# Optimization experiments

Measured on AMD Instinct MI355X. Metric: run time of the kernel, lower is better.

Reference implementation:

```python
import jax, jax.numpy as jnp
import numpy as np

STRIDE = 1
PADDING = 1  # zeros padding mode

def setup_inputs() -> dict:
    key = jax.random.key(0)
    k1, k2, k3 = jax.random.split(key, 3)
    N, C_in, H, W = 32, 128, 56, 56
    C_out, kH, kW = 256, 3, 3
    x = jax.random.normal(k1, (N, C_in, H, W), dtype=jnp.float32)
    fan_in = C_in * kH * kW
    weight = jax.random.normal(k2, (C_out, C_in, kH, kW), dtype=jnp.float32) / np.sqrt(fan_in)
    bias = jax.random.normal(k3, (C_out,), dtype=jnp.float32) * 0.01
    return {"x": x, "weight": weight, "bias": bias}

def reference(x, weight, bias):
    # Same math as the im2col unfold + GEMM: a standard 2D cross-correlation
    # with zero padding. Expressed as the fused implicit-GEMM conv primitive.
    out = jax.lax.conv_general_dilated(
        x, weight,
        window_strides=(STRIDE, STRIDE),
        padding=[(PADDING, PADDING), (PADDING, PADDING)],
        dimension_numbers=("NCHW", "OIHW", "NCHW"),
    )
    # bias broadcast over (N, C_out, H_out, W_out)
    return out + bias[None, :, None, None]
```

## Files before the change

### kernel.cpp

```cpp
#include <hip/hip_runtime.h>


typedef __attribute__((ext_vector_type(8))) short short8;
typedef __attribute__((ext_vector_type(4))) float float4v;

constexpr int NB = 32, CI = 128, HH = 56, WW = 56, CO = 256;
constexpr int HWP = HH * WW;
constexpr int M_TOTAL = NB * HWP;
constexpr size_t XT_BYTES = (size_t)NB * HWP * CI * 2;
constexpr size_t WT_BYTES = (size_t)9 * CO * CI * 2;
constexpr size_t ZP_OFF   = XT_BYTES + WT_BYTES;
constexpr size_t WS_NEED  = ZP_OFF + 128;

__device__ inline ushort f2bf(float v) {
    union { float f; uint u; } c; c.f = v;
    uint u = c.u;
    return (ushort)((u + 0x7fffu + ((u >> 16) & 1u)) >> 16);
}

__global__ __launch_bounds__(256) void xform_x(const float* __restrict__ x,
                                               ushort* __restrict__ xT) {
    int b = blockIdx.x;
    int cit = b & 3;
    int hwt = (b >> 2) % 49;
    int n   = b / (4 * 49);
    int ci0 = cit * 32, hw0 = hwt * 64;
    __shared__ float t[32][65];
    int tx = threadIdx.x;
    int col = tx & 63, r4 = tx >> 6;
#pragma unroll
    for (int rr = 0; rr < 8; ++rr) {
        int row = rr * 4 + r4;
        t[row][col] = x[((size_t)n * CI + ci0 + row) * HWP + hw0 + col];
    }
    __syncthreads();
    int i = tx & 31, j0 = tx >> 5;
#pragma unroll
    for (int jj = 0; jj < 8; ++jj) {
        int j = jj * 8 + j0;
        xT[((size_t)n * HWP + hw0 + j) * CI + ci0 + i] = f2bf(t[i][j]);
    }
}

__global__ __launch_bounds__(256) void xform_w(const float* __restrict__ w,
                                               ushort* __restrict__ wT) {
    int o = blockIdx.x * 256 + threadIdx.x;
    int ci = o & 127;
    int co = (o >> 7) & 255;
    int tap = o >> 15;
    wT[o] = f2bf(w[((size_t)co * CI + ci) * 9 + tap]);
}

__global__ __launch_bounds__(256) void gemm_conv(
    const ushort* __restrict__ xT, const ushort* __restrict__ wT,
    const ushort* __restrict__ zp, const float* __restrict__ bias,
    float* __restrict__ out)
{
    __shared__ ushort As[128 * 64];
    __shared__ ushort Bs[128 * 64];

    const int mblk = blockIdx.x >> 1;
    const int cblk = blockIdx.x & 1;
    const int tid = threadIdx.x, lane = tid & 63, wv = tid >> 6;
    const int wco = wv >> 1, wm = wv & 1;
    const int s = (lane & 7) ^ ((lane >> 3) & 7);

    int ho_[4], wo_[4], mpix[4], rowW[4];
#pragma unroll
    for (int q = 0; q < 4; ++q) {
        int r = wv * 32 + q * 8 + (lane >> 3);
        rowW[q] = r;
        int m = mblk * 128 + r;
        mpix[q] = m;
        int hw = m % HWP;
        ho_[q] = hw / WW;
        wo_[q] = hw % WW;
    }

    float4v acc[4][4];
#pragma unroll
    for (int i = 0; i < 4; ++i)
#pragma unroll
        for (int j = 0; j < 4; ++j) acc[i][j] = (float4v)(0.0f);

    for (int tap = 0; tap < 9; ++tap) {
        const int dh = tap / 3 - 1, dw = tap % 3 - 1;
        for (int cb = 0; cb < 2; ++cb) {
#pragma unroll
            for (int q = 0; q < 4; ++q) {
                const ushort* g = wT + ((size_t)tap * CO + cblk * 128 + rowW[q]) * CI
                                     + cb * 64 + s * 8;
                __builtin_amdgcn_global_load_lds(
                    (const __attribute__((address_space(1))) uint*)g,
                    (__attribute__((address_space(3))) uint*)(As + (wv * 32 + q * 8) * 64),
                    16, 0, 0);
            }
#pragma unroll
            for (int q = 0; q < 4; ++q) {
                int hi = ho_[q] + dh, wi = wo_[q] + dw;
                bool ok = (hi >= 0) & (hi < HH) & (wi >= 0) & (wi < WW);
                const ushort* g = ok
                    ? (xT + ((size_t)(mpix[q] + dh * WW + dw)) * CI + cb * 64 + s * 8)
                    : (zp + (lane & 7) * 8);
                __builtin_amdgcn_global_load_lds(
                    (const __attribute__((address_space(1))) uint*)g,
                    (__attribute__((address_space(3))) uint*)(Bs + (wv * 32 + q * 8) * 64),
                    16, 0, 0);
            }
            __syncthreads();
#pragma unroll
            for (int kk = 0; kk < 2; ++kk) {
                short8 a[4], b[4];
#pragma unroll
                for (int f = 0; f < 4; ++f) {
                    int row = wco * 64 + f * 16 + (lane & 15);
                    int ch = (kk * 4 + (lane >> 4)) ^ (row & 7);
                    a[f] = *(const short8*)(As + row * 64 + ch * 8);
                }
#pragma unroll
                for (int f = 0; f < 4; ++f) {
                    int row = wm * 64 + f * 16 + (lane & 15);
                    int ch = (kk * 4 + (lane >> 4)) ^ (row & 7);
                    b[f] = *(const short8*)(Bs + row * 64 + ch * 8);
                }
#pragma unroll
                for (int i = 0; i < 4; ++i)
#pragma unroll
                    for (int j = 0; j < 4; ++j)
                        acc[i][j] = __builtin_amdgcn_mfma_f32_16x16x32_bf16(
                            a[i], b[j], acc[i][j], 0, 0, 0);
            }
            __syncthreads();
        }
    }

    const int co0 = cblk * 128 + wco * 64;
    const int m0  = mblk * 128 + wm * 64;
    float bv[4][4];
#pragma unroll
    for (int i = 0; i < 4; ++i)
#pragma unroll
        for (int r = 0; r < 4; ++r)
            bv[i][r] = bias[co0 + i * 16 + (lane >> 4) * 4 + r];
#pragma unroll
    for (int j = 0; j < 4; ++j) {
        int m = m0 + j * 16 + (lane & 15);
        int n = m / HWP, hw = m % HWP;
        float* obase = out + (size_t)n * CO * HWP + hw;
#pragma unroll
        for (int i = 0; i < 4; ++i) {
            int co = co0 + i * 16 + (lane >> 4) * 4;
#pragma unroll
            for (int r = 0; r < 4; ++r)
                obase[(size_t)(co + r) * HWP] = acc[i][j][r] + bv[i][r];
        }
    }
}

__global__ __launch_bounds__(256) void conv_k(
    const float* __restrict__ x, const float* __restrict__ wgt,
    const float* __restrict__ bias, float* __restrict__ out)
{
    int idx = blockIdx.x * 256 + threadIdx.x;
    int wg = idx % 14; int t = idx / 14;
    int ho = t % 56; t /= 56;
    int cog = t % 64; int n = t / 64;
    int w0 = wg * 4, co0 = cog * 4;
    float acc[4][4];
#pragma unroll
    for (int j = 0; j < 4; ++j) {
        float bj = bias[co0 + j];
#pragma unroll
        for (int p = 0; p < 4; ++p) acc[j][p] = bj;
    }
    const float* xn = x + (size_t)n * CI * HWP;
    for (int ci = 0; ci < CI; ++ci) {
        float xr[3][6];
#pragma unroll
        for (int kh = 0; kh < 3; ++kh) {
            int hi = ho + kh - 1;
            if (hi >= 0 && hi < HH) {
                const float* row = xn + ((size_t)ci * HH + hi) * WW;
                float4 c = *reinterpret_cast<const float4*>(row + w0);
                xr[kh][1] = c.x; xr[kh][2] = c.y; xr[kh][3] = c.z; xr[kh][4] = c.w;
                xr[kh][0] = (w0 > 0) ? row[w0 - 1] : 0.0f;
                xr[kh][5] = (w0 + 4 < WW) ? row[w0 + 4] : 0.0f;
            } else {
#pragma unroll
                for (int q = 0; q < 6; ++q) xr[kh][q] = 0.0f;
            }
        }
#pragma unroll
        for (int j = 0; j < 4; ++j) {
            const float* wp = wgt + ((size_t)(co0 + j) * CI + ci) * 9;
            float wvv[9];
#pragma unroll
            for (int q = 0; q < 9; ++q) wvv[q] = wp[q];
#pragma unroll
            for (int kh = 0; kh < 3; ++kh)
#pragma unroll
                for (int kw = 0; kw < 3; ++kw)
#pragma unroll
                    for (int p = 0; p < 4; ++p)
                        acc[j][p] = fmaf(xr[kh][p + kw], wvv[kh * 3 + kw], acc[j][p]);
        }
    }
#pragma unroll
    for (int j = 0; j < 4; ++j) {
        float4 v = make_float4(acc[j][0], acc[j][1], acc[j][2], acc[j][3]);
        *reinterpret_cast<float4*>(out + (((size_t)n * CO + co0 + j) * HH + ho) * WW + w0) = v;
    }
}

extern "C" void kernel_launch(void* const* d_in, const int* in_sizes, int n_in,
                              void* d_out, int out_size, void* d_ws, size_t ws_size,
                              hipStream_t stream) {
    const float* x = (const float*)d_in[0];
    const float* w = (const float*)d_in[1];
    const float* b = (const float*)d_in[2];
    float* out = (float*)d_out;

    if (ws_size < WS_NEED) {
        hipLaunchKernelGGL(conv_k, dim3(6272), dim3(256), 0, stream, x, w, b, out);
        return;
    }

    ushort* xT = (ushort*)d_ws;
    ushort* wT = (ushort*)((char*)d_ws + XT_BYTES);
    ushort* zp = (ushort*)((char*)d_ws + ZP_OFF);

    hipMemsetAsync(zp, 0, 128, stream);
    hipLaunchKernelGGL(xform_x, dim3(32 * 49 * 4), dim3(256), 0, stream, x, xT);
    hipLaunchKernelGGL(xform_w, dim3(9 * CO * CI / 256), dim3(256), 0, stream, w, wT);
    hipLaunchKernelGGL(gemm_conv, dim3(784 * 2), dim3(256), 0, stream,
                       xT, wT, zp, b, out);
}
```

Before: 104.6 us.

## Pre-pad input in NHWC bf16 layout and remap block order for cache locality

The transposed bf16 input is now written into a zero-bordered 58x58 buffer, and a new kernel zeroes that border. The GEMM loop can then drop its per-tap bounds checks and zero-page fallback, using precomputed offsets instead. The block index is also remapped so each group of 8 consecutive blocks is strided across the grid, and the loops are reordered to iterate taps inside channel halves. These changes cost one extra small launch and a slightly larger workspace, and the remap may affect L2 reuse of neighbouring pixel rows.

```diff
diff --git a/kernel.cpp b/kernel.cpp
--- a/kernel.cpp
+++ b/kernel.cpp
@@ -6,11 +6,11 @@
 
 constexpr int NB = 32, CI = 128, HH = 56, WW = 56, CO = 256;
 constexpr int HWP = HH * WW;
-constexpr int M_TOTAL = NB * HWP;
-constexpr size_t XT_BYTES = (size_t)NB * HWP * CI * 2;
-constexpr size_t WT_BYTES = (size_t)9 * CO * CI * 2;
-constexpr size_t ZP_OFF   = XT_BYTES + WT_BYTES;
-constexpr size_t WS_NEED  = ZP_OFF + 128;
+constexpr int HP = 58, WP = 58;
+constexpr size_t XTP_BYTES = (size_t)NB * HP * WP * CI * 2;
+constexpr size_t WT_OFF    = XTP_BYTES;
+constexpr size_t WT_BYTES  = (size_t)9 * CO * CI * 2;
+constexpr size_t WS_NEED   = WT_OFF + WT_BYTES;
 
 __device__ inline ushort f2bf(float v) {
     union { float f; uint u; } c; c.f = v;
@@ -19,7 +19,7 @@
 }
 
 __global__ __launch_bounds__(256) void xform_x(const float* __restrict__ x,
-                                               ushort* __restrict__ xT) {
+                                               ushort* __restrict__ xTp) {
     int b = blockIdx.x;
     int cit = b & 3;
     int hwt = (b >> 2) % 49;
@@ -38,8 +38,23 @@
 #pragma unroll
     for (int jj = 0; jj < 8; ++jj) {
         int j = jj * 8 + j0;
-        xT[((size_t)n * HWP + hw0 + j) * CI + ci0 + i] = f2bf(t[i][j]);
-    }
+        int hw = hw0 + j;
+        int h = hw / WW, w = hw % WW;
+        xTp[(((size_t)n * HP + h + 1) * WP + (w + 1)) * CI + ci0 + i] = f2bf(t[i][j]);
+    }
+}
+
+__global__ __launch_bounds__(256) void xform_border(ushort* __restrict__ xTp) {
+    int u = blockIdx.x * 256 + threadIdx.x;
+    int ci8 = u & 15;
+    int r = u >> 4;
+    int n = r / 228, bb = r % 228;
+    int hp, wp;
+    if (bb < 58)       { hp = 0;  wp = bb; }
+    else if (bb < 116) { hp = 57; wp = bb - 58; }
+    else { int c = bb - 116; hp = 1 + (c >> 1); wp = (c & 1) * 57; }
+    short8 z = (short8)0;
+    *reinterpret_cast<short8*>(xTp + (((size_t)n * HP + hp) * WP + wp) * CI + ci8 * 8) = z;
 }
 
 __global__ __launch_bounds__(256) void xform_w(const float* __restrict__ w,
@@ -52,29 +67,29 @@
 }
 
 __global__ __launch_bounds__(256) void gemm_conv(
-    const ushort* __restrict__ xT, const ushort* __restrict__ wT,
-    const ushort* __restrict__ zp, const float* __restrict__ bias,
-    float* __restrict__ out)
+    const ushort* __restrict__ xTp, const ushort* __restrict__ wT,
+    const float* __restrict__ bias, float* __restrict__ out)
 {
     __shared__ ushort As[128 * 64];
     __shared__ ushort Bs[128 * 64];
 
-    const int mblk = blockIdx.x >> 1;
-    const int cblk = blockIdx.x & 1;
+    int b = blockIdx.x;
+    int logical = (b & 7) * 196 + (b >> 3);
+    const int mblk = logical >> 1;
+    const int cblk = logical & 1;
+
     const int tid = threadIdx.x, lane = tid & 63, wv = tid >> 6;
     const int wco = wv >> 1, wm = wv & 1;
     const int s = (lane & 7) ^ ((lane >> 3) & 7);
 
-    int ho_[4], wo_[4], mpix[4], rowW[4];
+    int aOff[4], bOff[4];
 #pragma unroll
     for (int q = 0; q < 4; ++q) {
         int r = wv * 32 + q * 8 + (lane >> 3);
-        rowW[q] = r;
+        aOff[q] = (cblk * 128 + r) * CI + s * 8;
         int m = mblk * 128 + r;
-        mpix[q] = m;
-        int hw = m % HWP;
-        ho_[q] = hw / WW;
-        wo_[q] = hw % WW;
+        int n = m / HWP, hw = m % HWP, h = hw / WW, w = hw % WW;
+        bOff[q] = ((n * HP + h + 1) * WP + (w + 1)) * CI + s * 8;
     }
 
     float4v acc[4][4];
@@ -83,34 +98,30 @@
 #pragma unroll
         for (int j = 0; j < 4; ++j) acc[i][j] = (float4v)(0.0f);
 
-    for (int tap = 0; tap < 9; ++tap) {
-        const int dh = tap / 3 - 1, dw = tap % 3 - 1;
-        for (int cb = 0; cb < 2; ++cb) {
+    for (int cb = 0; cb < 2; ++cb) {
+#pragma unroll 1
+        for (int tap = 0; tap < 9; ++tap) {
+            const int dh = tap / 3 - 1, dw = tap % 3 - 1;
+            const int toff = (dh * WP + dw) * CI + cb * 64;
+            const int atap = tap * CO * CI + cb * 64;
 #pragma unroll
             for (int q = 0; q < 4; ++q) {
-                const ushort* g = wT + ((size_t)tap * CO + cblk * 128 + rowW[q]) * CI
-                                     + cb * 64 + s * 8;
                 __builtin_amdgcn_global_load_lds(
-                    (const __attribute__((address_space(1))) uint*)g,
+                    (const __attribute__((address_space(1))) uint*)(wT + aOff[q] + atap),
                     (__attribute__((address_space(3))) uint*)(As + (wv * 32 + q * 8) * 64),
                     16, 0, 0);
             }
 #pragma unroll
             for (int q = 0; q < 4; ++q) {
-                int hi = ho_[q] + dh, wi = wo_[q] + dw;
-                bool ok = (hi >= 0) & (hi < HH) & (wi >= 0) & (wi < WW);
-                const ushort* g = ok
-                    ? (xT + ((size_t)(mpix[q] + dh * WW + dw)) * CI + cb * 64 + s * 8)
-                    : (zp + (lane & 7) * 8);
                 __builtin_amdgcn_global_load_lds(
-                    (const __attribute__((address_space(1))) uint*)g,
+                    (const __attribute__((address_space(1))) uint*)(xTp + bOff[q] + toff),
                     (__attribute__((address_space(3))) uint*)(Bs + (wv * 32 + q * 8) * 64),
                     16, 0, 0);
             }
             __syncthreads();
 #pragma unroll
             for (int kk = 0; kk < 2; ++kk) {
-                short8 a[4], b[4];
+                short8 a[4], bfr[4];
 #pragma unroll
                 for (int f = 0; f < 4; ++f) {
                     int row = wco * 64 + f * 16 + (lane & 15);
@@ -121,14 +132,14 @@
                 for (int f = 0; f < 4; ++f) {
                     int row = wm * 64 + f * 16 + (lane & 15);
                     int ch = (kk * 4 + (lane >> 4)) ^ (row & 7);
-                    b[f] = *(const short8*)(Bs + row * 64 + ch * 8);
+                    bfr[f] = *(const short8*)(Bs + row * 64 + ch * 8);
                 }
 #pragma unroll
                 for (int i = 0; i < 4; ++i)
 #pragma unroll
                     for (int j = 0; j < 4; ++j)
                         acc[i][j] = __builtin_amdgcn_mfma_f32_16x16x32_bf16(
-                            a[i], b[j], acc[i][j], 0, 0, 0);
+                            a[i], bfr[j], acc[i][j], 0, 0, 0);
             }
             __syncthreads();
         }
@@ -225,13 +236,12 @@
         return;
     }
 
-    ushort* xT = (ushort*)d_ws;
-    ushort* wT = (ushort*)((char*)d_ws + XT_BYTES);
-    ushort* zp = (ushort*)((char*)d_ws + ZP_OFF);
-
-    hipMemsetAsync(zp, 0, 128, stream);
-    hipLaunchKernelGGL(xform_x, dim3(32 * 49 * 4), dim3(256), 0, stream, x, xT);
+    ushort* xTp = (ushort*)d_ws;
+    ushort* wT  = (ushort*)((char*)d_ws + WT_OFF);
+
+    hipLaunchKernelGGL(xform_x, dim3(32 * 49 * 4), dim3(256), 0, stream, x, xTp);
+    hipLaunchKernelGGL(xform_border, dim3(456), dim3(256), 0, stream, xTp);
     hipLaunchKernelGGL(xform_w, dim3(9 * CO * CI / 256), dim3(256), 0, stream, w, wT);
     hipLaunchKernelGGL(gemm_conv, dim3(784 * 2), dim3(256), 0, stream,
-                       xT, wT, zp, b, out);
-}
+                       xTp, wT, b, out);
+}
```

After: 108.1 us. +3.4%, slower.
